# Kernel optimization log

Measured on AMD Instinct MI355X. Metric: run time of the kernel, lower is better.

## Reference

```python
import jax, jax.numpy as jnp
import numpy as np

B, T, C = 4, 2048, 1024
N_HEAD = 16
HEAD_DIM = C // N_HEAD


def setup_inputs() -> dict:
    key = jax.random.key(0)
    k1, k2, k3 = jax.random.split(key, 3)
    x = jax.random.normal(k1, (B, T, C), dtype=jnp.float32)
    W_attn = jax.random.normal(k2, (C, 3 * C), dtype=jnp.float32) * (1.0 / np.sqrt(C))
    b_attn = jnp.zeros((3 * C,), dtype=jnp.float32)
    W_proj = jax.random.normal(k3, (C, C), dtype=jnp.float32) * (1.0 / np.sqrt(C))
    b_proj = jnp.zeros((C,), dtype=jnp.float32)
    return {"x": x, "W_attn": W_attn, "b_attn": b_attn, "W_proj": W_proj, "b_proj": b_proj}


def reference(x, W_attn, b_attn, W_proj, b_proj):
    Bx, Tx, Cx = x.shape
    qkv = x @ W_attn + b_attn  # (B,T,3C)
    q, k, v = jnp.split(qkv, 3, axis=-1)
    # (B, n_head, T, head_dim)
    def to_heads(t):
        return t.reshape(Bx, Tx, N_HEAD, HEAD_DIM).transpose(0, 2, 1, 3)
    q, k, v = to_heads(q), to_heads(k), to_heads(v)
    scale = 1.0 / np.sqrt(HEAD_DIM)
    scores = jnp.einsum('bhqd,bhkd->bhqk', q, k) * scale  # (B,H,T,T)
    causal = jnp.tril(jnp.ones((Tx, Tx), dtype=bool))
    scores = jnp.where(causal[None, None, :, :], scores, -jnp.inf)
    probs = jax.nn.softmax(scores, axis=-1)
    attn = jnp.einsum('bhqk,bhkd->bhqd', probs, v)  # (B,H,T,D)
    attn = attn.transpose(0, 2, 1, 3).reshape(Bx, Tx, Cx)
    return attn @ W_proj + b_proj
```

## Files before the change

### kernel.cpp

```cpp
#include <hip/hip_runtime.h>


typedef __attribute__((ext_vector_type(8))) __bf16 bf16x8;
typedef __attribute__((ext_vector_type(4))) float f32x4;
typedef __attribute__((ext_vector_type(4))) short s16x4;

__device__ __forceinline__ unsigned short f2bf(float f) {
    unsigned u = __builtin_bit_cast(unsigned, f);
    u += 0x7fffu + ((u >> 16) & 1u);
    return (unsigned short)(u >> 16);
}
__device__ __forceinline__ unsigned pack2bf(float a, float b) {
    return (unsigned)f2bf(a) | ((unsigned)f2bf(b) << 16);
}
__device__ __forceinline__ void gload16(const unsigned short* g, unsigned short* l) {
    __builtin_amdgcn_global_load_lds(
        (const __attribute__((address_space(1))) unsigned int*)g,
        (__attribute__((address_space(3))) unsigned int*)l, 16, 0, 0);
}

__global__ void convert_kernel(const float* __restrict__ in, unsigned short* __restrict__ out,
                               long n) {
    long i = ((long)blockIdx.x * blockDim.x + threadIdx.x) * 4;
    if (i >= n) return;
    f32x4 v = *reinterpret_cast<const f32x4*>(&in[i]);
    s16x4 o;
    o[0] = (short)f2bf(v[0]);
    o[1] = (short)f2bf(v[1]);
    o[2] = (short)f2bf(v[2]);
    o[3] = (short)f2bf(v[3]);
    *reinterpret_cast<s16x4*>(&out[i]) = o;
}

__global__ void transpose_kernel(const float* __restrict__ Wa, unsigned short* __restrict__ Wta,
                                 const float* __restrict__ Wp, unsigned short* __restrict__ Wtp) {
    __shared__ float t[32][33];
    const int tid = threadIdx.x;
    int bx = blockIdx.x;
    const float* W;
    unsigned short* Wt;
    int N;
    if (bx < 96) { W = Wa; Wt = Wta; N = 3072; }
    else         { W = Wp; Wt = Wtp; N = 1024; bx -= 96; }
    const int K = 1024;
    const int n0 = bx * 32, k0 = blockIdx.y * 32;
    const int row = tid >> 3, c4 = (tid & 7) * 4;
    f32x4 v = *reinterpret_cast<const f32x4*>(&W[(size_t)(k0 + row) * N + n0 + c4]);
    t[row][c4 + 0] = v[0];
    t[row][c4 + 1] = v[1];
    t[row][c4 + 2] = v[2];
    t[row][c4 + 3] = v[3];
    __syncthreads();
    s16x4 o;
    o[0] = (short)f2bf(t[c4 + 0][row]);
    o[1] = (short)f2bf(t[c4 + 1][row]);
    o[2] = (short)f2bf(t[c4 + 2][row]);
    o[3] = (short)f2bf(t[c4 + 3][row]);
    *reinterpret_cast<s16x4*>(&Wt[(size_t)(n0 + row) * K + k0 + c4]) = o;
}

template <int MODE>
__global__ __launch_bounds__(256, 2)
void gemm_kernel(const unsigned short* __restrict__ A,
                 const unsigned short* __restrict__ Bt,
                 const float* __restrict__ bias,
                 float* __restrict__ Cout,
                 unsigned short* __restrict__ Qo,
                 unsigned short* __restrict__ Ko,
                 unsigned short* __restrict__ Vto,
                 int M, int N, int Kd) {
    __shared__ unsigned short As[128 * 64];
    __shared__ unsigned short Bs[128 * 64];
    const int tid = threadIdx.x;
    const int wave = tid >> 6, lane = tid & 63;
    const int l15 = lane & 15, lhi = lane >> 4;
    const int wm = wave >> 1, wn = wave & 1;
    const int m0 = blockIdx.x * 128, n0 = blockIdx.y * 128;

    f32x4 acc[4][4];
#pragma unroll
    for (int i = 0; i < 4; i++)
#pragma unroll
        for (int j = 0; j < 4; j++) acc[i][j] = f32x4{0.f, 0.f, 0.f, 0.f};

    const int r0 = tid >> 3;
    const int cswz = (((tid & 7) ^ (r0 & 7)) << 3);
    const unsigned short* Ap = &A[(size_t)(m0 + r0) * Kd + cswz];
    const unsigned short* Bp = &Bt[(size_t)(n0 + r0) * Kd + cswz];
    const size_t K32 = (size_t)32 * Kd;
    const int csw0 = (lhi * 8) ^ ((l15 & 7) << 3);

    for (int k0 = 0; k0 < Kd; k0 += 64) {
#pragma unroll
        for (int blk = 0; blk < 4; blk++) {
            gload16(Ap + blk * K32 + k0, &As[blk * 2048 + tid * 8]);
            gload16(Bp + blk * K32 + k0, &Bs[blk * 2048 + tid * 8]);
        }
        __syncthreads();

        bf16x8 av[2][4], bv[2][4];
#pragma unroll
        for (int ks = 0; ks < 2; ks++)
#pragma unroll
            for (int i = 0; i < 4; i++) {
                av[ks][i] = *reinterpret_cast<const bf16x8*>(
                    &As[(wm * 64 + i * 16 + l15) * 64 + (ks * 32 ^ csw0)]);
                bv[ks][i] = *reinterpret_cast<const bf16x8*>(
                    &Bs[(wn * 64 + i * 16 + l15) * 64 + (ks * 32 ^ csw0)]);
            }
#pragma unroll
        for (int ks = 0; ks < 2; ks++)
#pragma unroll
            for (int i = 0; i < 4; i++)
#pragma unroll
                for (int j = 0; j < 4; j++)
                    acc[i][j] = __builtin_amdgcn_mfma_f32_16x16x32_bf16(av[ks][i], bv[ks][j],
                                                                        acc[i][j], 0, 0, 0);
        __syncthreads();
    }

#pragma unroll
    for (int j = 0; j < 4; j++) {
        const int col = n0 + wn * 64 + j * 16 + l15;
        const float bv = bias[col];
#pragma unroll
        for (int i = 0; i < 4; i++) {
            const int rbase = m0 + wm * 64 + i * 16 + lhi * 4;
#pragma unroll
            for (int r = 0; r < 4; r++) {
                const int row = rbase + r;
                const float oval = acc[i][j][r] + bv;
                if (MODE == 0) {
                    Cout[(size_t)row * N + col] = oval;
                } else {
                    const int sel = col >> 10, c1 = col & 1023;
                    const int h = c1 >> 6, d = c1 & 63;
                    const int b = row >> 11, t = row & 2047;
                    if (sel == 0)
                        Qo[(((size_t)(b * 16 + h)) * 2048 + t) * 64 + d] = f2bf(oval * 0.125f);
                    else if (sel == 1)
                        Ko[(((size_t)(b * 16 + h)) * 2048 + t) * 64 + d] = f2bf(oval);
                    else
                        Vto[(((size_t)(b * 16 + h)) * 64 + d) * 2048 + t] = f2bf(oval);
                }
            }
        }
    }
}

__global__ __launch_bounds__(256, 2)
void attn_kernel(const unsigned short* __restrict__ Q,
                 const unsigned short* __restrict__ Kg,
                 const unsigned short* __restrict__ Vt,
                 unsigned short* __restrict__ Aout) {
    __shared__ unsigned int Pl[4][16 * 36];
    const int tid = threadIdx.x, wave = tid >> 6, lane = tid & 63;
    const int l15 = lane & 15, lhi = lane >> 4;
    const int bid = blockIdx.x;
    const int head = bid & 63;
    const int j = bid >> 6;
    const int qb = (j < 4) ? j : (11 - j);
    const int q0w = qb * 256 + wave * 64;
    const unsigned short* Qh = Q + (size_t)head * (2048 * 64);
    const unsigned short* Kh = Kg + (size_t)head * (2048 * 64);
    const unsigned short* Vh = Vt + (size_t)head * (64 * 2048);
    unsigned int* P = &Pl[wave][0];

    bf16x8 qfr[4][2];
#pragma unroll
    for (int qf = 0; qf < 4; qf++)
#pragma unroll
        for (int dh = 0; dh < 2; dh++)
            qfr[qf][dh] = *reinterpret_cast<const bf16x8*>(
                &Qh[(size_t)(q0w + qf * 16 + l15) * 64 + dh * 32 + lhi * 8]);

    f32x4 o[4][4];
#pragma unroll
    for (int df = 0; df < 4; df++)
#pragma unroll
        for (int qf = 0; qf < 4; qf++) o[df][qf] = f32x4{0.f, 0.f, 0.f, 0.f};
    float m[4] = {-1e30f, -1e30f, -1e30f, -1e30f};
    float l[4] = {0.f, 0.f, 0.f, 0.f};

#define LOADK(DST, kt)                                                                  \
    do {                                                                                \
        _Pragma("unroll") for (int kf = 0; kf < 4; kf++)                                \
            _Pragma("unroll") for (int dh = 0; dh < 2; dh++)                            \
                DST[kf][dh] = *reinterpret_cast<const bf16x8*>(                         \
                    &Kh[(size_t)((kt) + kf * 16 + l15) * 64 + dh * 32 + lhi * 8]);      \
    } while (0)

    const int ntiles = (q0w >> 6) + 1;
    bf16x8 ka[4][2], kb[4][2], vfr[4][2];
    LOADK(ka, 0);
    for (int t = 0; t < ntiles; ++t) {
        const int kt = t * 64;
        const bool masked = (t == ntiles - 1);
#pragma unroll
        for (int df = 0; df < 4; df++)
#pragma unroll
            for (int kc = 0; kc < 2; kc++)
                vfr[df][kc] = *reinterpret_cast<const bf16x8*>(
                    &Vh[(size_t)(df * 16 + l15) * 2048 + kt + kc * 32 + lhi * 8]);
        const int ktn = masked ? kt : kt + 64;
        LOADK(kb, ktn);

#pragma unroll
        for (int qf = 0; qf < 4; qf++) {
            f32x4 s[4];
#pragma unroll
            for (int kf = 0; kf < 4; kf++) {
                s[kf] = __builtin_amdgcn_mfma_f32_16x16x32_bf16(ka[kf][0], qfr[qf][0],
                                                                f32x4{0.f, 0.f, 0.f, 0.f}, 0, 0, 0);
                s[kf] = __builtin_amdgcn_mfma_f32_16x16x32_bf16(ka[kf][1], qfr[qf][1], s[kf], 0, 0, 0);
            }
            if (masked) {
#pragma unroll
                for (int kf = 0; kf < 4; kf++)
#pragma unroll
                    for (int r = 0; r < 4; r++)
                        if (kf * 16 + lhi * 4 + r > qf * 16 + l15) s[kf][r] = -1e30f;
            }
            float tm = s[0][0];
#pragma unroll
            for (int kf = 0; kf < 4; kf++)
#pragma unroll
                for (int r = 0; r < 4; r++) tm = fmaxf(tm, s[kf][r]);
            tm = fmaxf(tm, __shfl_xor(tm, 16));
            tm = fmaxf(tm, __shfl_xor(tm, 32));
            const float mn = fmaxf(m[qf], tm);
            const float corr = __expf(m[qf] - mn);
            m[qf] = mn;
            float rs = 0.f;
#pragma unroll
            for (int kf = 0; kf < 4; kf++)
#pragma unroll
                for (int r = 0; r < 4; r++) {
                    const float p = __expf(s[kf][r] - mn);
                    s[kf][r] = p;
                    rs += p;
                }
            rs += __shfl_xor(rs, 16);
            rs += __shfl_xor(rs, 32);
            l[qf] = l[qf] * corr + rs;
#pragma unroll
            for (int df = 0; df < 4; df++)
#pragma unroll
                for (int r = 0; r < 4; r++) o[df][qf][r] *= corr;

#pragma unroll
            for (int kf = 0; kf < 4; kf++) {
                P[l15 * 36 + kf * 8 + lhi * 2 + 0] = pack2bf(s[kf][0], s[kf][1]);
                P[l15 * 36 + kf * 8 + lhi * 2 + 1] = pack2bf(s[kf][2], s[kf][3]);
            }
            asm volatile("s_waitcnt lgkmcnt(0)" ::: "memory");
            bf16x8 pb0 = *reinterpret_cast<const bf16x8*>(&P[l15 * 36 + 0 * 16 + lhi * 4]);
            bf16x8 pb1 = *reinterpret_cast<const bf16x8*>(&P[l15 * 36 + 1 * 16 + lhi * 4]);
#pragma unroll
            for (int df = 0; df < 4; df++) {
                o[df][qf] = __builtin_amdgcn_mfma_f32_16x16x32_bf16(vfr[df][0], pb0, o[df][qf], 0, 0, 0);
                o[df][qf] = __builtin_amdgcn_mfma_f32_16x16x32_bf16(vfr[df][1], pb1, o[df][qf], 0, 0, 0);
            }
        }
#pragma unroll
        for (int kf = 0; kf < 4; kf++)
#pragma unroll
            for (int dh = 0; dh < 2; dh++) ka[kf][dh] = kb[kf][dh];
    }
#undef LOADK

    const int b = head >> 4, h = head & 15;
#pragma unroll
    for (int qf = 0; qf < 4; qf++) {
        const float inv = 1.0f / l[qf];
        unsigned short* op = Aout + ((size_t)(b * 2048 + q0w + qf * 16 + l15)) * 1024 + h * 64;
#pragma unroll
        for (int df = 0; df < 4; df++) {
            *reinterpret_cast<unsigned*>(&op[df * 16 + lhi * 4]) =
                pack2bf(o[df][qf][0] * inv, o[df][qf][1] * inv);
            *reinterpret_cast<unsigned*>(&op[df * 16 + lhi * 4 + 2]) =
                pack2bf(o[df][qf][2] * inv, o[df][qf][3] * inv);
        }
    }
}

extern "C" void kernel_launch(void* const* d_in, const int* in_sizes, int n_in,
                              void* d_out, int out_size, void* d_ws, size_t ws_size,
                              hipStream_t stream) {
    const float* x     = (const float*)d_in[0];
    const float* Wattn = (const float*)d_in[1];
    const float* battn = (const float*)d_in[2];
    const float* Wproj = (const float*)d_in[3];
    const float* bproj = (const float*)d_in[4];
    float* out = (float*)d_out;

    unsigned short* ws = (unsigned short*)d_ws;
    const size_t HS = (size_t)4 * 16 * 2048 * 64;
    unsigned short* Qb  = ws;
    unsigned short* Kb  = Qb + HS;
    unsigned short* Vtb = Kb + HS;
    unsigned short* Ab  = Vtb + HS;
    unsigned short* Wta = Ab + HS;
    unsigned short* Wtp = Wta + (size_t)3072 * 1024;
    unsigned short* xb  = Wtp + (size_t)1024 * 1024;

    convert_kernel<<<8192, 256, 0, stream>>>(x, xb, (long)HS);
    transpose_kernel<<<dim3(128, 32), 256, 0, stream>>>(Wattn, Wta, Wproj, Wtp);
    gemm_kernel<1><<<dim3(64, 24), 256, 0, stream>>>(xb, Wta, battn, nullptr, Qb, Kb, Vtb,
                                                     8192, 3072, 1024);
    attn_kernel<<<512, 256, 0, stream>>>(Qb, Kb, Vtb, Ab);
    gemm_kernel<0><<<dim3(64, 8), 256, 0, stream>>>(Ab, Wtp, bproj, out, nullptr, nullptr, nullptr,
                                                    8192, 1024, 1024);
}
```

Measured before the change: 197.5 us.

## Use 512-thread GEMM blocks with 4x2 wave grid and K-step of 32

The GEMM kernel goes from 256 to 512 threads per block, split across a 2x4 wave grid where each wave computes a 64x32 sub-tile. The K tile shrinks from 64 to 32, so each iteration does one 16-byte global-to-LDS load per matrix per thread and uses a new 4-way XOR swizzle. The intent is more waves to hide latency and less shared memory per block. The cost is twice as many K-iterations, each with two barriers, and fewer MFMAs per barrier, which may increase synchronisation overhead.

```diff
diff --git a/kernel.cpp b/kernel.cpp
--- a/kernel.cpp
+++ b/kernel.cpp
@@ -60,7 +60,7 @@
 }
 
 template <int MODE>
-__global__ __launch_bounds__(256, 2)
+__global__ __launch_bounds__(512, 2)
 void gemm_kernel(const unsigned short* __restrict__ A,
                  const unsigned short* __restrict__ Bt,
                  const float* __restrict__ bias,
@@ -69,59 +69,49 @@
                  unsigned short* __restrict__ Ko,
                  unsigned short* __restrict__ Vto,
                  int M, int N, int Kd) {
-    __shared__ unsigned short As[128 * 64];
-    __shared__ unsigned short Bs[128 * 64];
+    __shared__ unsigned short As[128 * 32];
+    __shared__ unsigned short Bs[128 * 32];
     const int tid = threadIdx.x;
     const int wave = tid >> 6, lane = tid & 63;
     const int l15 = lane & 15, lhi = lane >> 4;
-    const int wm = wave >> 1, wn = wave & 1;
+    const int wm = wave >> 2, wn = wave & 3;
     const int m0 = blockIdx.x * 128, n0 = blockIdx.y * 128;
 
-    f32x4 acc[4][4];
+    f32x4 acc[4][2];
 #pragma unroll
     for (int i = 0; i < 4; i++)
 #pragma unroll
-        for (int j = 0; j < 4; j++) acc[i][j] = f32x4{0.f, 0.f, 0.f, 0.f};
-
-    const int r0 = tid >> 3;
-    const int cswz = (((tid & 7) ^ (r0 & 7)) << 3);
-    const unsigned short* Ap = &A[(size_t)(m0 + r0) * Kd + cswz];
-    const unsigned short* Bp = &Bt[(size_t)(n0 + r0) * Kd + cswz];
-    const size_t K32 = (size_t)32 * Kd;
-    const int csw0 = (lhi * 8) ^ ((l15 & 7) << 3);
-
-    for (int k0 = 0; k0 < Kd; k0 += 64) {
-#pragma unroll
-        for (int blk = 0; blk < 4; blk++) {
-            gload16(Ap + blk * K32 + k0, &As[blk * 2048 + tid * 8]);
-            gload16(Bp + blk * K32 + k0, &Bs[blk * 2048 + tid * 8]);
-        }
+        for (int j = 0; j < 2; j++) acc[i][j] = f32x4{0.f, 0.f, 0.f, 0.f};
+
+    const int r0 = tid >> 2;
+    const int ca = (((tid & 3) ^ (r0 & 3)) << 3);
+    const unsigned short* Ap = &A[(size_t)(m0 + r0) * Kd + ca];
+    const unsigned short* Bp = &Bt[(size_t)(n0 + r0) * Kd + ca];
+    const int csw = ((lhi ^ (l15 & 3)) << 3);
+
+    for (int k0 = 0; k0 < Kd; k0 += 32) {
+        gload16(Ap + k0, &As[tid * 8]);
+        gload16(Bp + k0, &Bs[tid * 8]);
         __syncthreads();
 
-        bf16x8 av[2][4], bv[2][4];
-#pragma unroll
-        for (int ks = 0; ks < 2; ks++)
-#pragma unroll
-            for (int i = 0; i < 4; i++) {
-                av[ks][i] = *reinterpret_cast<const bf16x8*>(
-                    &As[(wm * 64 + i * 16 + l15) * 64 + (ks * 32 ^ csw0)]);
-                bv[ks][i] = *reinterpret_cast<const bf16x8*>(
-                    &Bs[(wn * 64 + i * 16 + l15) * 64 + (ks * 32 ^ csw0)]);
-            }
-#pragma unroll
-        for (int ks = 0; ks < 2; ks++)
-#pragma unroll
-            for (int i = 0; i < 4; i++)
-#pragma unroll
-                for (int j = 0; j < 4; j++)
-                    acc[i][j] = __builtin_amdgcn_mfma_f32_16x16x32_bf16(av[ks][i], bv[ks][j],
-                                                                        acc[i][j], 0, 0, 0);
+        bf16x8 av[4], bv[2];
+#pragma unroll
+        for (int i = 0; i < 4; i++)
+            av[i] = *reinterpret_cast<const bf16x8*>(&As[(wm * 64 + i * 16 + l15) * 32 + csw]);
+#pragma unroll
+        for (int j = 0; j < 2; j++)
+            bv[j] = *reinterpret_cast<const bf16x8*>(&Bs[(wn * 32 + j * 16 + l15) * 32 + csw]);
+#pragma unroll
+        for (int i = 0; i < 4; i++)
+#pragma unroll
+            for (int j = 0; j < 2; j++)
+                acc[i][j] = __builtin_amdgcn_mfma_f32_16x16x32_bf16(av[i], bv[j], acc[i][j], 0, 0, 0);
         __syncthreads();
     }
 
 #pragma unroll
-    for (int j = 0; j < 4; j++) {
-        const int col = n0 + wn * 64 + j * 16 + l15;
+    for (int j = 0; j < 2; j++) {
+        const int col = n0 + wn * 32 + j * 16 + l15;
         const float bv = bias[col];
 #pragma unroll
         for (int i = 0; i < 4; i++) {
@@ -306,9 +296,9 @@
 
     convert_kernel<<<8192, 256, 0, stream>>>(x, xb, (long)HS);
     transpose_kernel<<<dim3(128, 32), 256, 0, stream>>>(Wattn, Wta, Wproj, Wtp);
-    gemm_kernel<1><<<dim3(64, 24), 256, 0, stream>>>(xb, Wta, battn, nullptr, Qb, Kb, Vtb,
+    gemm_kernel<1><<<dim3(64, 24), 512, 0, stream>>>(xb, Wta, battn, nullptr, Qb, Kb, Vtb,
                                                      8192, 3072, 1024);
     attn_kernel<<<512, 256, 0, stream>>>(Qb, Kb, Vtb, Ab);
-    gemm_kernel<0><<<dim3(64, 8), 256, 0, stream>>>(Ab, Wtp, bproj, out, nullptr, nullptr, nullptr,
+    gemm_kernel<0><<<dim3(64, 8), 512, 0, stream>>>(Ab, Wtp, bproj, out, nullptr, nullptr, nullptr,
                                                     8192, 1024, 1024);
 }
```

New measurement: 216.0 us. 1.09x slower.

## Enlarge GEMM M-tile to 256 and merge convert/transpose into one prep kernel

Applied to the files above, without the earlier changes.

Each GEMM workgroup now computes a 256x128 output tile instead of 128x128, with each wave holding 8x4 accumulators. This raises operand reuse per LDS load and halves the grid in the M dimension. The separate x-convert and weight-transpose kernels are folded into a single launch to save one launch. The cost is more registers per thread and fewer workgroups: 768 for QKV and 256 for the projection, which may leave CUs underfilled given the launch_bounds of 2 waves per SIMD.

```diff
diff --git a/kernel.cpp b/kernel.cpp
--- a/kernel.cpp
+++ b/kernel.cpp
@@ -19,31 +19,32 @@
         (__attribute__((address_space(3))) unsigned int*)l, 16, 0, 0);
 }
 
-__global__ void convert_kernel(const float* __restrict__ in, unsigned short* __restrict__ out,
-                               long n) {
-    long i = ((long)blockIdx.x * blockDim.x + threadIdx.x) * 4;
-    if (i >= n) return;
-    f32x4 v = *reinterpret_cast<const f32x4*>(&in[i]);
-    s16x4 o;
-    o[0] = (short)f2bf(v[0]);
-    o[1] = (short)f2bf(v[1]);
-    o[2] = (short)f2bf(v[2]);
-    o[3] = (short)f2bf(v[3]);
-    *reinterpret_cast<s16x4*>(&out[i]) = o;
-}
-
-__global__ void transpose_kernel(const float* __restrict__ Wa, unsigned short* __restrict__ Wta,
-                                 const float* __restrict__ Wp, unsigned short* __restrict__ Wtp) {
+__global__ void prep_kernel(const float* __restrict__ x, unsigned short* __restrict__ xb,
+                            const float* __restrict__ Wa, unsigned short* __restrict__ Wta,
+                            const float* __restrict__ Wp, unsigned short* __restrict__ Wtp) {
     __shared__ float t[32][33];
     const int tid = threadIdx.x;
-    int bx = blockIdx.x;
+    const int bid = blockIdx.x;
+    if (bid < 8192) {
+        long i = ((long)bid * 256 + tid) * 4;
+        f32x4 v = *reinterpret_cast<const f32x4*>(&x[i]);
+        s16x4 o;
+        o[0] = (short)f2bf(v[0]);
+        o[1] = (short)f2bf(v[1]);
+        o[2] = (short)f2bf(v[2]);
+        o[3] = (short)f2bf(v[3]);
+        *reinterpret_cast<s16x4*>(&xb[i]) = o;
+        return;
+    }
+    int tb = bid - 8192;
+    int bx = tb & 127, by = tb >> 7;
     const float* W;
     unsigned short* Wt;
     int N;
     if (bx < 96) { W = Wa; Wt = Wta; N = 3072; }
     else         { W = Wp; Wt = Wtp; N = 1024; bx -= 96; }
     const int K = 1024;
-    const int n0 = bx * 32, k0 = blockIdx.y * 32;
+    const int n0 = bx * 32, k0 = by * 32;
     const int row = tid >> 3, c4 = (tid & 7) * 4;
     f32x4 v = *reinterpret_cast<const f32x4*>(&W[(size_t)(k0 + row) * N + n0 + c4]);
     t[row][c4 + 0] = v[0];
@@ -69,17 +70,17 @@
                  unsigned short* __restrict__ Ko,
                  unsigned short* __restrict__ Vto,
                  int M, int N, int Kd) {
-    __shared__ unsigned short As[128 * 64];
+    __shared__ unsigned short As[256 * 64];
     __shared__ unsigned short Bs[128 * 64];
     const int tid = threadIdx.x;
     const int wave = tid >> 6, lane = tid & 63;
     const int l15 = lane & 15, lhi = lane >> 4;
     const int wm = wave >> 1, wn = wave & 1;
-    const int m0 = blockIdx.x * 128, n0 = blockIdx.y * 128;
-
-    f32x4 acc[4][4];
-#pragma unroll
-    for (int i = 0; i < 4; i++)
+    const int m0 = blockIdx.x * 256, n0 = blockIdx.y * 128;
+
+    f32x4 acc[8][4];
+#pragma unroll
+    for (int i = 0; i < 8; i++)
 #pragma unroll
         for (int j = 0; j < 4; j++) acc[i][j] = f32x4{0.f, 0.f, 0.f, 0.f};
 
@@ -92,30 +93,31 @@
 
     for (int k0 = 0; k0 < Kd; k0 += 64) {
 #pragma unroll
-        for (int blk = 0; blk < 4; blk++) {
+        for (int blk = 0; blk < 8; blk++)
             gload16(Ap + blk * K32 + k0, &As[blk * 2048 + tid * 8]);
+#pragma unroll
+        for (int blk = 0; blk < 4; blk++)
             gload16(Bp + blk * K32 + k0, &Bs[blk * 2048 + tid * 8]);
+        __syncthreads();
+
+#pragma unroll
+        for (int ks = 0; ks < 2; ks++) {
+            bf16x8 av[8], bv[4];
+#pragma unroll
+            for (int i = 0; i < 8; i++)
+                av[i] = *reinterpret_cast<const bf16x8*>(
+                    &As[(wm * 128 + i * 16 + l15) * 64 + (ks * 32 ^ csw0)]);
+#pragma unroll
+            for (int j = 0; j < 4; j++)
+                bv[j] = *reinterpret_cast<const bf16x8*>(
+                    &Bs[(wn * 64 + j * 16 + l15) * 64 + (ks * 32 ^ csw0)]);
+#pragma unroll
+            for (int i = 0; i < 8; i++)
+#pragma unroll
+                for (int j = 0; j < 4; j++)
+                    acc[i][j] = __builtin_amdgcn_mfma_f32_16x16x32_bf16(av[i], bv[j],
+                                                                        acc[i][j], 0, 0, 0);
         }
-        __syncthreads();
-
-        bf16x8 av[2][4], bv[2][4];
-#pragma unroll
-        for (int ks = 0; ks < 2; ks++)
-#pragma unroll
-            for (int i = 0; i < 4; i++) {
-                av[ks][i] = *reinterpret_cast<const bf16x8*>(
-                    &As[(wm * 64 + i * 16 + l15) * 64 + (ks * 32 ^ csw0)]);
-                bv[ks][i] = *reinterpret_cast<const bf16x8*>(
-                    &Bs[(wn * 64 + i * 16 + l15) * 64 + (ks * 32 ^ csw0)]);
-            }
-#pragma unroll
-        for (int ks = 0; ks < 2; ks++)
-#pragma unroll
-            for (int i = 0; i < 4; i++)
-#pragma unroll
-                for (int j = 0; j < 4; j++)
-                    acc[i][j] = __builtin_amdgcn_mfma_f32_16x16x32_bf16(av[ks][i], bv[ks][j],
-                                                                        acc[i][j], 0, 0, 0);
         __syncthreads();
     }
 
@@ -124,8 +126,8 @@
         const int col = n0 + wn * 64 + j * 16 + l15;
         const float bv = bias[col];
 #pragma unroll
-        for (int i = 0; i < 4; i++) {
-            const int rbase = m0 + wm * 64 + i * 16 + lhi * 4;
+        for (int i = 0; i < 8; i++) {
+            const int rbase = m0 + wm * 128 + i * 16 + lhi * 4;
 #pragma unroll
             for (int r = 0; r < 4; r++) {
                 const int row = rbase + r;
@@ -304,11 +306,10 @@
     unsigned short* Wtp = Wta + (size_t)3072 * 1024;
     unsigned short* xb  = Wtp + (size_t)1024 * 1024;
 
-    convert_kernel<<<8192, 256, 0, stream>>>(x, xb, (long)HS);
-    transpose_kernel<<<dim3(128, 32), 256, 0, stream>>>(Wattn, Wta, Wproj, Wtp);
-    gemm_kernel<1><<<dim3(64, 24), 256, 0, stream>>>(xb, Wta, battn, nullptr, Qb, Kb, Vtb,
+    prep_kernel<<<12288, 256, 0, stream>>>(x, xb, Wattn, Wta, Wproj, Wtp);
+    gemm_kernel<1><<<dim3(32, 24), 256, 0, stream>>>(xb, Wta, battn, nullptr, Qb, Kb, Vtb,
                                                      8192, 3072, 1024);
     attn_kernel<<<512, 256, 0, stream>>>(Qb, Kb, Vtb, Ab);
-    gemm_kernel<0><<<dim3(64, 8), 256, 0, stream>>>(Ab, Wtp, bproj, out, nullptr, nullptr, nullptr,
+    gemm_kernel<0><<<dim3(32, 8), 256, 0, stream>>>(Ab, Wtp, bproj, out, nullptr, nullptr, nullptr,
                                                     8192, 1024, 1024);
 }
```

Result: slower. 215.5 us (+9.1%).
